# Kernel tuning notes

Hardware: AMD Instinct MI355X
Metric: run time of the kernel (lower is better)

Reference implementation:

```python
import jax, jax.numpy as jnp
import numpy as np
from jax import lax

B, CIN, COUT, H, W = 4, 32, 64, 192, 192
K = 3  # kernel size
RED = 16  # SE reduction
EPS = 1e-5


def _conv2d_same(x, w, b):
    y = lax.conv_general_dilated(x, w, (1, 1), 'SAME',
                                 dimension_numbers=('NCHW', 'OIHW', 'NCHW'))
    return y + b[None, :, None, None]


def _bilinear_gather(x, py, px):
    # x: [B,C,H,W]; py/px: [B,KK,H,W] absolute sample coords -> [B,C,KK,H,W]
    Bb, C, Hh, Ww = x.shape
    KK = py.shape[1]
    y0 = jnp.floor(py); x0 = jnp.floor(px)
    wy = py - y0; wx = px - x0
    x_flat = x.reshape(Bb, C, Hh * Ww)

    def corner(yi, xi, wgt):
        valid = (yi >= 0) & (yi < Hh) & (xi >= 0) & (xi < Ww)
        yc = jnp.clip(yi, 0, Hh - 1).astype(jnp.int32)
        xc = jnp.clip(xi, 0, Ww - 1).astype(jnp.int32)
        idx = (yc * Ww + xc).reshape(Bb, 1, KK * Hh * Ww)
        g = jnp.take_along_axis(x_flat, idx, axis=2).reshape(Bb, C, KK, Hh, Ww)
        w_eff = (wgt * valid.astype(x.dtype))[:, None]  # [B,1,KK,H,W]
        return g * w_eff

    out = (corner(y0, x0, (1 - wy) * (1 - wx))
           + corner(y0, x0 + 1, (1 - wy) * wx)
           + corner(y0 + 1, x0, wy * (1 - wx))
           + corner(y0 + 1, x0 + 1, wy * wx))
    return out  # [B,C,KK,H,W]


def _deform_conv(x, offsets, w, b):
    # torchvision DeformConv2d, stride 1, pad 1, dilation 1, 1 offset group.
    Bb, C, Hh, Ww = x.shape
    off = offsets.reshape(Bb, K * K, 2, Hh, Ww)
    dy, dx = off[:, :, 0], off[:, :, 1]  # [B,KK,H,W]
    ky, kx = jnp.meshgrid(jnp.arange(K) - 1, jnp.arange(K) - 1, indexing='ij')
    hg, wg = jnp.meshgrid(jnp.arange(Hh), jnp.arange(Ww), indexing='ij')
    py = hg[None, None] + ky.reshape(-1)[None, :, None, None] + dy
    px = wg[None, None] + kx.reshape(-1)[None, :, None, None] + dx
    sampled = _bilinear_gather(x, py, px)  # [B,CIN,KK,H,W]
    y = jnp.einsum('bckhw,ock->bohw', sampled, w.reshape(w.shape[0], C, K * K))
    return y + b[None, :, None, None]


def _forward(x, w_off, b_off, w_def, b_def, bn_gamma, bn_beta,
             fc1_w, fc1_b, fc2_w, fc2_b):
    offsets = _conv2d_same(x, w_off, b_off)
    y = _deform_conv(x, offsets, w_def, b_def)
    # BatchNorm2d (training-mode batch statistics)
    mean = jnp.mean(y, axis=(0, 2, 3), keepdims=True)
    var = jnp.var(y, axis=(0, 2, 3), keepdims=True)
    y = (y - mean) * lax.rsqrt(var + EPS)
    y = y * bn_gamma[None, :, None, None] + bn_beta[None, :, None, None]
    # SE layer
    s = jnp.mean(y, axis=(2, 3))  # [B,C]
    s = jax.nn.relu(s @ fc1_w.T + fc1_b)
    s = jax.nn.sigmoid(s @ fc2_w.T + fc2_b)
    y = y * s[:, :, None, None]
    y = jax.nn.relu(y)
    # MaxPool 2x2 stride 2
    y = lax.reduce_window(y, -jnp.inf, lax.max, (1, 1, 2, 2), (1, 1, 2, 2), 'VALID')
    return y


def setup_inputs() -> dict:
    key = jax.random.key(0)
    ks = jax.random.split(key, 12)
    rn = lambda k, s, sc=1.0: (jax.random.normal(k, s, dtype=jnp.float32) * sc)
    return {
        'x': rn(ks[0], (B, CIN, H, W)),
        'w_off': rn(ks[1], (2 * K * K, CIN, K, K), 0.02),
        'b_off': jnp.zeros((2 * K * K,), jnp.float32),
        'w_def': rn(ks[2], (COUT, CIN, K, K), 0.05),
        'b_def': rn(ks[3], (COUT,), 0.05),
        'bn_gamma': jnp.ones((COUT,), jnp.float32),
        'bn_beta': jnp.zeros((COUT,), jnp.float32),
        'fc1_w': rn(ks[4], (COUT // RED, COUT), 0.1),
        'fc1_b': jnp.zeros((COUT // RED,), jnp.float32),
        'fc2_w': rn(ks[5], (COUT, COUT // RED), 0.1),
        'fc2_b': jnp.zeros((COUT,), jnp.float32),
    }


def reference(x, w_off, b_off, w_def, b_def, bn_gamma, bn_beta,
              fc1_w, fc1_b, fc2_w, fc2_b):
    return _forward(x, w_off, b_off, w_def, b_def, bn_gamma, bn_beta,
                    fc1_w, fc1_b, fc2_w, fc2_b)
```

## Files before the change

### kernel.cpp

```cpp
#include <hip/hip_runtime.h>
#include <math.h>

#define B_    4
#define CIN_  32
#define COUT_ 64
#define H_    192
#define W_    192
#define HW_   (H_ * W_)
#define NPIX_ (B_ * HW_)
#define EPS_  1e-5f

static __device__ __forceinline__ int swz2304(int blk) {
    return ((blk & 7) * 288) + (blk >> 3);
}

struct Cr { int o00, o01, o10, o11; float w00, w01, w10, w11; };

__global__ __launch_bounds__(256) void k_pre(
    const float* __restrict__ x, const float* __restrict__ w_def,
    const float* __restrict__ w_off, float* __restrict__ xt,
    float* __restrict__ wt_def, float* __restrict__ wt_off,
    float* __restrict__ stats)
{
    if (blockIdx.x < NPIX_ / 256) {
        __shared__ float lds[32 * 257];
        const int tid  = threadIdx.x;
        const int pid0 = blockIdx.x * 256;
        const int b    = pid0 / HW_;
        const int rem0 = pid0 - b * HW_;
        const float* xb = x + (size_t)b * CIN_ * HW_ + rem0;

#pragma unroll
        for (int c = 0; c < 32; ++c)
            lds[c * 257 + tid] = xb[c * HW_ + tid];
        __syncthreads();

        float4* dst = (float4*)(xt + (size_t)pid0 * 32);
#pragma unroll
        for (int i = 0; i < 8; ++i) {
            const int idx = i * 256 + tid;
            const int px  = idx >> 3;
            const int q   = idx & 7;
            float4 v;
            v.x = lds[(q * 4 + 0) * 257 + px];
            v.y = lds[(q * 4 + 1) * 257 + px];
            v.z = lds[(q * 4 + 2) * 257 + px];
            v.w = lds[(q * 4 + 3) * 257 + px];
            dst[idx] = v;
        }
    } else {
        const int i = (blockIdx.x - NPIX_ / 256) * 256 + threadIdx.x;
        if (i < 18432) {
            const int o  = i & 63;
            const int c  = (i >> 6) & 31;
            const int kk = i >> 11;
            wt_def[i] = w_def[(o * 32 + c) * 9 + kk];
        } else if (i < 18432 + 5760) {
            const int e  = i - 18432;
            const int c  = e & 31;
            const int t  = e >> 5;
            const int o  = t % 20;
            const int kk = t / 20;
            wt_off[e] = (o < 18) ? w_off[(o * 32 + c) * 9 + kk] : 0.f;
        } else if (i < 18432 + 5760 + 512) {
            stats[i - 18432 - 5760] = 0.f;
        }
    }
}

__global__ __launch_bounds__(256, 6) void k_fused(
    const float* __restrict__ xt, const float* __restrict__ wto,
    const float* __restrict__ b_off, const float* __restrict__ wtd,
    const float* __restrict__ b_def, float* __restrict__ y,
    float* __restrict__ sum_bc, float* __restrict__ sumsq_bc)
{
    __shared__ __align__(16) float smem[6336];
    __shared__ float offlds[20 * 64];
    float4 (*tile)[198] = (float4(*)[198])smem;
    float* vbuf = smem;

    const int tid  = threadIdx.x;
    const int px   = tid & 63;
    const int og   = __builtin_amdgcn_readfirstlane(tid >> 6);
    const int lane = tid & 63;

    const int blk  = swz2304(blockIdx.x);
    const int base = blk * 64;
    const int b    = base / HW_;
    const int rem0 = base - b * HW_;
    const int h0   = rem0 / W_;
    const int w0   = rem0 - h0 * W_;
    const float* xb = xt + (size_t)b * HW_ * 32;

    for (int i = tid; i < 1584; i += 256) {
        const int j   = i & 7;
        const int rec = i >> 3;
        const int r   = rec / 66;
        const int cc  = rec - r * 66;
        const int hc  = min(max(h0 + r - 1, 0), H_ - 1);
        const int wc  = min(max(w0 + cc - 1, 0), W_ - 1);
        tile[j][rec] = *(const float4*)(xb + (hc * W_ + wc) * 32 + j * 4);
    }
    __syncthreads();

    {
        const bool rv0 = (h0 - 1 >= 0), rv2 = (h0 + 1 < H_);
        float acc5[5] = {0.f, 0.f, 0.f, 0.f, 0.f};
#pragma unroll 1
        for (int kk = 0; kk < 9; ++kk) {
            const int ky = kk / 3, kx = kk % 3;
            const bool rok = (ky == 0) ? rv0 : ((ky == 2) ? rv2 : true);
            const int wcol = w0 + px + kx - 1;
            const float g = (rok && wcol >= 0 && wcol < W_) ? 1.f : 0.f;
            const int rec = ky * 66 + px + kx;

            float4 v[8];
#pragma unroll
            for (int j = 0; j < 8; ++j) {
                v[j] = tile[j][rec];
                v[j].x *= g; v[j].y *= g; v[j].z *= g; v[j].w *= g;
            }
            const float* wk = wto + (kk * 20 + og * 5) * 32;
#pragma unroll
            for (int oo = 0; oo < 5; ++oo) {
                const float4* wr = (const float4*)(wk + oo * 32);
                float s = acc5[oo];
#pragma unroll
                for (int j = 0; j < 8; ++j) {
                    const float4 wv = wr[j];
                    s += v[j].x * wv.x + v[j].y * wv.y
                       + v[j].z * wv.z + v[j].w * wv.w;
                }
                acc5[oo] = s;
            }
        }
#pragma unroll
        for (int oo = 0; oo < 5; ++oo) {
            const int o = og * 5 + oo;
            if (o < 18) offlds[o * 64 + px] = acc5[oo] + b_off[o];
        }
    }
    __syncthreads();

    const int h = h0;
    const int w = w0 + px;
    const float* xg = xb + og * 8;

    float acc[16];
#pragma unroll
    for (int q = 0; q < 16; ++q) acc[q] = 0.f;

    auto mk = [&](int kk) -> Cr {
        const float dy = offlds[(2 * kk) * 64 + px];
        const float dx = offlds[(2 * kk + 1) * 64 + px];
        const float py = (float)(h + kk / 3 - 1) + dy;
        const float qx = (float)(w + kk % 3 - 1) + dx;
        const float y0f = floorf(py), x0f = floorf(qx);
        const float wy = py - y0f, wx = qx - x0f;
        const int iy0 = (int)y0f, ix0 = (int)x0f;
        const int iy1 = iy0 + 1,  ix1 = ix0 + 1;
        const float vy0 = (iy0 >= 0 && iy0 < H_) ? 1.f : 0.f;
        const float vy1 = (iy1 >= 0 && iy1 < H_) ? 1.f : 0.f;
        const float vx0 = (ix0 >= 0 && ix0 < W_) ? 1.f : 0.f;
        const float vx1 = (ix1 >= 0 && ix1 < W_) ? 1.f : 0.f;
        Cr c;
        c.w00 = (1.f - wy) * (1.f - wx) * vy0 * vx0;
        c.w01 = (1.f - wy) * wx * vy0 * vx1;
        c.w10 = wy * (1.f - wx) * vy1 * vx0;
        c.w11 = wy * wx * vy1 * vx1;
        const int cy0 = min(max(iy0, 0), H_ - 1), cy1 = min(max(iy1, 0), H_ - 1);
        const int cx0 = min(max(ix0, 0), W_ - 1), cx1 = min(max(ix1, 0), W_ - 1);
        c.o00 = (cy0 * W_ + cx0) * 32; c.o01 = (cy0 * W_ + cx1) * 32;
        c.o10 = (cy1 * W_ + cx0) * 32; c.o11 = (cy1 * W_ + cx1) * 32;
        return c;
    };

    {
        Cr c0 = mk(0);
        float4 A0 = *(const float4*)(xg + c0.o00), A1 = *(const float4*)(xg + c0.o00 + 4);
        float4 B0 = *(const float4*)(xg + c0.o01), B1 = *(const float4*)(xg + c0.o01 + 4);
        float4 C0 = *(const float4*)(xg + c0.o10), C1 = *(const float4*)(xg + c0.o10 + 4);
        float4 D0 = *(const float4*)(xg + c0.o11), D1 = *(const float4*)(xg + c0.o11 + 4);
        float v[8];
        v[0] = c0.w00 * A0.x + c0.w01 * B0.x + c0.w10 * C0.x + c0.w11 * D0.x;
        v[1] = c0.w00 * A0.y + c0.w01 * B0.y + c0.w10 * C0.y + c0.w11 * D0.y;
        v[2] = c0.w00 * A0.z + c0.w01 * B0.z + c0.w10 * C0.z + c0.w11 * D0.z;
        v[3] = c0.w00 * A0.w + c0.w01 * B0.w + c0.w10 * C0.w + c0.w11 * D0.w;
        v[4] = c0.w00 * A1.x + c0.w01 * B1.x + c0.w10 * C1.x + c0.w11 * D1.x;
        v[5] = c0.w00 * A1.y + c0.w01 * B1.y + c0.w10 * C1.y + c0.w11 * D1.y;
        v[6] = c0.w00 * A1.z + c0.w01 * B1.z + c0.w10 * C1.z + c0.w11 * D1.z;
        v[7] = c0.w00 * A1.w + c0.w01 * B1.w + c0.w10 * C1.w + c0.w11 * D1.w;
#pragma unroll
        for (int j = 0; j < 8; ++j) vbuf[(og * 8 + j) * 64 + px] = v[j];
    }
    __syncthreads();

#pragma unroll 1
    for (int kk = 0; kk < 9; ++kk) {
        Cr nx; float4 A0, A1, B0, B1, C0, C1, D0, D1;
        if (kk < 8) {
            nx = mk(kk + 1);
            A0 = *(const float4*)(xg + nx.o00); A1 = *(const float4*)(xg + nx.o00 + 4);
            B0 = *(const float4*)(xg + nx.o01); B1 = *(const float4*)(xg + nx.o01 + 4);
            C0 = *(const float4*)(xg + nx.o10); C1 = *(const float4*)(xg + nx.o10 + 4);
            D0 = *(const float4*)(xg + nx.o11); D1 = *(const float4*)(xg + nx.o11 + 4);
        }

        const float* vp = vbuf + (kk & 1) * 2048;
        const float* wk = wtd + (kk << 11) + (og << 4);
#pragma unroll 8
        for (int c = 0; c < 32; ++c) {
            const float vv = vp[c * 64 + px];
            const float4* wr = (const float4*)(wk + (c << 6));
            const float4 w0 = wr[0], w1 = wr[1], w2 = wr[2], w3 = wr[3];
            acc[ 0] += vv * w0.x; acc[ 1] += vv * w0.y;
            acc[ 2] += vv * w0.z; acc[ 3] += vv * w0.w;
            acc[ 4] += vv * w1.x; acc[ 5] += vv * w1.y;
            acc[ 6] += vv * w1.z; acc[ 7] += vv * w1.w;
            acc[ 8] += vv * w2.x; acc[ 9] += vv * w2.y;
            acc[10] += vv * w2.z; acc[11] += vv * w2.w;
            acc[12] += vv * w3.x; acc[13] += vv * w3.y;
            acc[14] += vv * w3.z; acc[15] += vv * w3.w;
        }

        if (kk < 8) {
            float v[8];
            v[0] = nx.w00 * A0.x + nx.w01 * B0.x + nx.w10 * C0.x + nx.w11 * D0.x;
            v[1] = nx.w00 * A0.y + nx.w01 * B0.y + nx.w10 * C0.y + nx.w11 * D0.y;
            v[2] = nx.w00 * A0.z + nx.w01 * B0.z + nx.w10 * C0.z + nx.w11 * D0.z;
            v[3] = nx.w00 * A0.w + nx.w01 * B0.w + nx.w10 * C0.w + nx.w11 * D0.w;
            v[4] = nx.w00 * A1.x + nx.w01 * B1.x + nx.w10 * C1.x + nx.w11 * D1.x;
            v[5] = nx.w00 * A1.y + nx.w01 * B1.y + nx.w10 * C1.y + nx.w11 * D1.y;
            v[6] = nx.w00 * A1.z + nx.w01 * B1.z + nx.w10 * C1.z + nx.w11 * D1.z;
            v[7] = nx.w00 * A1.w + nx.w01 * B1.w + nx.w10 * C1.w + nx.w11 * D1.w;
            float* wp = vbuf + ((kk + 1) & 1) * 2048;
#pragma unroll
            for (int j = 0; j < 8; ++j) wp[(og * 8 + j) * 64 + px] = v[j];
            __syncthreads();
        }
    }

    const int rem = rem0 + px;
    float* yp = y + ((size_t)b * COUT_ + og * 16) * HW_ + rem;
#pragma unroll
    for (int q = 0; q < 16; ++q) {
        acc[q] += b_def[og * 16 + q];
        yp[q * HW_] = acc[q];
    }

    float ls = 0.f, lq = 0.f;
#pragma unroll
    for (int o = 0; o < 16; ++o) {
        float t = acc[o];
        float u = t * t;
#pragma unroll
        for (int s = 32; s; s >>= 1) {
            t += __shfl_xor(t, s, 64);
            u += __shfl_xor(u, s, 64);
        }
        if (lane == o) { ls = t; lq = u; }
    }
    if (lane < 16) {
        atomicAdd(&sum_bc[b * 64 + og * 16 + lane], ls);
        atomicAdd(&sumsq_bc[b * 64 + og * 16 + lane], lq);
    }
}

__global__ __launch_bounds__(256) void k_finish(
    const float* __restrict__ y,
    const float* __restrict__ sum_bc, const float* __restrict__ sumsq_bc,
    const float* __restrict__ gamma, const float* __restrict__ beta,
    const float* __restrict__ fc1_w, const float* __restrict__ fc1_b,
    const float* __restrict__ fc2_w, const float* __restrict__ fc2_b,
    float* __restrict__ out)
{
    __shared__ float sal[256], sbb[256], sin_[256];
    const int tid = threadIdx.x;
    {
        const int b = tid >> 6, c = tid & 63;
        float ch_s = 0.f, ch_q = 0.f;
#pragma unroll
        for (int bb = 0; bb < 4; ++bb) {
            ch_s += sum_bc[bb * 64 + c];
            ch_q += sumsq_bc[bb * 64 + c];
        }
        const float invN = 1.f / (float)(B_ * HW_);
        const float mean = ch_s * invN;
        const float var  = ch_q * invN - mean * mean;
        const float a    = gamma[c] * rsqrtf(var + EPS_);
        const float bi   = beta[c] - mean * a;
        sin_[tid] = a * (sum_bc[tid] * (1.f / (float)HW_)) + bi;
        __syncthreads();
        float hv[4];
#pragma unroll
        for (int j = 0; j < 4; ++j) {
            float hs = fc1_b[j];
            for (int cc = 0; cc < 64; ++cc)
                hs += sin_[b * 64 + cc] * fc1_w[j * 64 + cc];
            hv[j] = fmaxf(hs, 0.f);
        }
        float o = fc2_b[c];
#pragma unroll
        for (int j = 0; j < 4; ++j) o += hv[j] * fc2_w[c * 4 + j];
        const float s = 1.f / (1.f + expf(-o));
        sal[tid] = a * s;
        sbb[tid] = bi * s;
    }
    __syncthreads();

    const int t    = blockIdx.x * 256 + tid;
    const int opix = t * 2;
    const int bc   = opix / (96 * 96);
    const int rem  = opix - bc * (96 * 96);
    const int oh   = rem / 96, ow = rem - oh * 96;
    const float al = sal[bc], bb = sbb[bc];
    const float* yp = y + (size_t)bc * HW_ + (2 * oh) * W_ + 2 * ow;
    const float4 r0 = *(const float4*)yp;
    const float4 r1 = *(const float4*)(yp + W_);
    float2 st;
    st.x = fmaxf(fmaxf(fmaxf(fmaf(r0.x, al, bb), fmaf(r0.y, al, bb)),
                       fmaxf(fmaf(r1.x, al, bb), fmaf(r1.y, al, bb))), 0.f);
    st.y = fmaxf(fmaxf(fmaxf(fmaf(r0.z, al, bb), fmaf(r0.w, al, bb)),
                       fmaxf(fmaf(r1.z, al, bb), fmaf(r1.w, al, bb))), 0.f);
    *(float2*)(out + opix) = st;
}

extern "C" void kernel_launch(void* const* d_in, const int* in_sizes, int n_in,
                              void* d_out, int out_size, void* d_ws, size_t ws_size,
                              hipStream_t stream)
{
    const float* x     = (const float*)d_in[0];
    const float* w_off = (const float*)d_in[1];
    const float* b_off = (const float*)d_in[2];
    const float* w_def = (const float*)d_in[3];
    const float* b_def = (const float*)d_in[4];
    const float* gamma = (const float*)d_in[5];
    const float* beta  = (const float*)d_in[6];
    const float* fc1_w = (const float*)d_in[7];
    const float* fc1_b = (const float*)d_in[8];
    const float* fc2_w = (const float*)d_in[9];
    const float* fc2_b = (const float*)d_in[10];
    float* out = (float*)d_out;

    float* ws   = (float*)d_ws;
    float* yb     = ws;
    float* xt     = yb + 9437184;
    float* wt_def = xt + 4718592;
    float* wt_off = wt_def + 18432;
    float* stats  = wt_off + 5760;
    float* sum_bc   = stats;
    float* sumsq_bc = stats + 256;

    k_pre   <<<dim3(NPIX_ / 256 + 97), dim3(256), 0, stream>>>(
                x, w_def, w_off, xt, wt_def, wt_off, stats);
    k_fused <<<dim3(NPIX_ / 64), dim3(256), 0, stream>>>(
                xt, wt_off, b_off, wt_def, b_def, yb, sum_bc, sumsq_bc);
    k_finish<<<dim3(B_ * COUT_ * 96 * 96 / 512), dim3(256), 0, stream>>>(
                yb, sum_bc, sumsq_bc, gamma, beta,
                fc1_w, fc1_b, fc2_w, fc2_b, out);
}
```

Baseline: 221.6 us.

## Compute deformable conv contraction with split-fp16 MFMA instead of scalar FMA

Replaces the per-thread scalar FMA loop over 32 channels × 16 outputs with MFMA 16x16x32 f16 instructions. Both activations and weights are split into hi/lo fp16 parts, and three products (hi·hi, lo·hi, hi·lo) are accumulated to keep near-fp32 accuracy. The work is remapped so each wavefront handles 16 pixels × 64 outputs with 8 channels per lane-quad. This removes the LDS double-buffer exchange of sampled values and the per-kk barriers. Each lane now gathers its own bilinear samples, with no software prefetch of the next tap. Occupancy is lowered to 4 blocks per CU, the statistics reduction is restructured, and weights are stored pre-swizzled in fp16 pairs.

```diff
diff --git a/kernel.cpp b/kernel.cpp
--- a/kernel.cpp
+++ b/kernel.cpp
@@ -10,16 +10,19 @@
 #define NPIX_ (B_ * HW_)
 #define EPS_  1e-5f
 
+typedef _Float16 half8 __attribute__((ext_vector_type(8)));
+typedef float    f32x4 __attribute__((ext_vector_type(4)));
+
+#define WTN_ 18432
+
 static __device__ __forceinline__ int swz2304(int blk) {
     return ((blk & 7) * 288) + (blk >> 3);
 }
-
-struct Cr { int o00, o01, o10, o11; float w00, w01, w10, w11; };
 
 __global__ __launch_bounds__(256) void k_pre(
     const float* __restrict__ x, const float* __restrict__ w_def,
     const float* __restrict__ w_off, float* __restrict__ xt,
-    float* __restrict__ wt_def, float* __restrict__ wt_off,
+    _Float16* __restrict__ wt_def, float* __restrict__ wt_off,
     float* __restrict__ stats)
 {
     if (blockIdx.x < NPIX_ / 256) {
@@ -50,34 +53,39 @@
         }
     } else {
         const int i = (blockIdx.x - NPIX_ / 256) * 256 + threadIdx.x;
-        if (i < 18432) {
-            const int o  = i & 63;
-            const int c  = (i >> 6) & 31;
+        if (i < WTN_) {
+            const int j  = i & 7;
+            const int ln = (i >> 3) & 63;
+            const int ot = (i >> 9) & 3;
             const int kk = i >> 11;
-            wt_def[i] = w_def[(o * 32 + c) * 9 + kk];
-        } else if (i < 18432 + 5760) {
-            const int e  = i - 18432;
+            const int o  = ot * 16 + (ln & 15);
+            const int c  = (ln >> 4) * 8 + j;
+            const float wv = w_def[(o * 32 + c) * 9 + kk];
+            const _Float16 hi = (_Float16)wv;
+            wt_def[i]        = hi;
+            wt_def[WTN_ + i] = (_Float16)(wv - (float)hi);
+        } else if (i < WTN_ + 5760) {
+            const int e  = i - WTN_;
             const int c  = e & 31;
             const int t  = e >> 5;
             const int o  = t % 20;
             const int kk = t / 20;
             wt_off[e] = (o < 18) ? w_off[(o * 32 + c) * 9 + kk] : 0.f;
-        } else if (i < 18432 + 5760 + 512) {
-            stats[i - 18432 - 5760] = 0.f;
-        }
-    }
-}
-
-__global__ __launch_bounds__(256, 6) void k_fused(
+        } else if (i < WTN_ + 5760 + 512) {
+            stats[i - WTN_ - 5760] = 0.f;
+        }
+    }
+}
+
+__global__ __launch_bounds__(256, 4) void k_fused(
     const float* __restrict__ xt, const float* __restrict__ wto,
-    const float* __restrict__ b_off, const float* __restrict__ wtd,
+    const float* __restrict__ b_off, const _Float16* __restrict__ wtd,
     const float* __restrict__ b_def, float* __restrict__ y,
     float* __restrict__ sum_bc, float* __restrict__ sumsq_bc)
 {
     __shared__ __align__(16) float smem[6336];
-    __shared__ float offlds[20 * 64];
     float4 (*tile)[198] = (float4(*)[198])smem;
-    float* vbuf = smem;
+    float* offlds = smem;
 
     const int tid  = threadIdx.x;
     const int px   = tid & 63;
@@ -103,9 +111,9 @@
     }
     __syncthreads();
 
+    float acc5[5] = {0.f, 0.f, 0.f, 0.f, 0.f};
     {
         const bool rv0 = (h0 - 1 >= 0), rv2 = (h0 + 1 < H_);
-        float acc5[5] = {0.f, 0.f, 0.f, 0.f, 0.f};
 #pragma unroll 1
         for (int kk = 0; kk < 9; ++kk) {
             const int ky = kk / 3, kx = kk % 3;
@@ -134,27 +142,44 @@
                 acc5[oo] = s;
             }
         }
-#pragma unroll
-        for (int oo = 0; oo < 5; ++oo) {
-            const int o = og * 5 + oo;
-            if (o < 18) offlds[o * 64 + px] = acc5[oo] + b_off[o];
-        }
     }
     __syncthreads();
-
-    const int h = h0;
-    const int w = w0 + px;
-    const float* xg = xb + og * 8;
-
-    float acc[16];
-#pragma unroll
-    for (int q = 0; q < 16; ++q) acc[q] = 0.f;
-
-    auto mk = [&](int kk) -> Cr {
-        const float dy = offlds[(2 * kk) * 64 + px];
-        const float dx = offlds[(2 * kk + 1) * 64 + px];
-        const float py = (float)(h + kk / 3 - 1) + dy;
-        const float qx = (float)(w + kk % 3 - 1) + dx;
+#pragma unroll
+    for (int oo = 0; oo < 5; ++oo) {
+        const int o = og * 5 + oo;
+        if (o < 18) offlds[o * 64 + px] = acc5[oo] + b_off[o];
+    }
+    __syncthreads();
+
+    const int l15 = lane & 15;
+    const int lq4 = lane >> 4;
+    const int pxl = (og << 4) + l15;
+    const int wc_ = w0 + pxl;
+    const float* xg = xb + lq4 * 8;
+    const _Float16* wbh = wtd + lane * 8;
+    const _Float16* wbl = wtd + WTN_ + lane * 8;
+
+    f32x4 acc[4];
+#pragma unroll
+    for (int ot = 0; ot < 4; ++ot) acc[ot] = (f32x4){0.f, 0.f, 0.f, 0.f};
+
+#pragma unroll 1
+    for (int kk = 0; kk < 9; ++kk) {
+        const _Float16* wkh = wbh + (kk << 11);
+        const _Float16* wkl = wbl + (kk << 11);
+        const half8 bh0 = *(const half8*)(wkh);
+        const half8 bh1 = *(const half8*)(wkh + 512);
+        const half8 bh2 = *(const half8*)(wkh + 1024);
+        const half8 bh3 = *(const half8*)(wkh + 1536);
+        const half8 bl0 = *(const half8*)(wkl);
+        const half8 bl1 = *(const half8*)(wkl + 512);
+        const half8 bl2 = *(const half8*)(wkl + 1024);
+        const half8 bl3 = *(const half8*)(wkl + 1536);
+
+        const float dy = offlds[(2 * kk) * 64 + pxl];
+        const float dx = offlds[(2 * kk + 1) * 64 + pxl];
+        const float py = (float)(h0 + kk / 3 - 1) + dy;
+        const float qx = (float)(wc_ + kk % 3 - 1) + dx;
         const float y0f = floorf(py), x0f = floorf(qx);
         const float wy = py - y0f, wx = qx - x0f;
         const int iy0 = (int)y0f, ix0 = (int)x0f;
@@ -163,107 +188,72 @@
         const float vy1 = (iy1 >= 0 && iy1 < H_) ? 1.f : 0.f;
         const float vx0 = (ix0 >= 0 && ix0 < W_) ? 1.f : 0.f;
         const float vx1 = (ix1 >= 0 && ix1 < W_) ? 1.f : 0.f;
-        Cr c;
-        c.w00 = (1.f - wy) * (1.f - wx) * vy0 * vx0;
-        c.w01 = (1.f - wy) * wx * vy0 * vx1;
-        c.w10 = wy * (1.f - wx) * vy1 * vx0;
-        c.w11 = wy * wx * vy1 * vx1;
+        const float w00 = (1.f - wy) * (1.f - wx) * vy0 * vx0;
+        const float w01 = (1.f - wy) * wx * vy0 * vx1;
+        const float w10 = wy * (1.f - wx) * vy1 * vx0;
+        const float w11 = wy * wx * vy1 * vx1;
         const int cy0 = min(max(iy0, 0), H_ - 1), cy1 = min(max(iy1, 0), H_ - 1);
         const int cx0 = min(max(ix0, 0), W_ - 1), cx1 = min(max(ix1, 0), W_ - 1);
-        c.o00 = (cy0 * W_ + cx0) * 32; c.o01 = (cy0 * W_ + cx1) * 32;
-        c.o10 = (cy1 * W_ + cx0) * 32; c.o11 = (cy1 * W_ + cx1) * 32;
-        return c;
-    };
-
-    {
-        Cr c0 = mk(0);
-        float4 A0 = *(const float4*)(xg + c0.o00), A1 = *(const float4*)(xg + c0.o00 + 4);
-        float4 B0 = *(const float4*)(xg + c0.o01), B1 = *(const float4*)(xg + c0.o01 + 4);
-        float4 C0 = *(const float4*)(xg + c0.o10), C1 = *(const float4*)(xg + c0.o10 + 4);
-        float4 D0 = *(const float4*)(xg + c0.o11), D1 = *(const float4*)(xg + c0.o11 + 4);
+        const int o00 = (cy0 * W_ + cx0) * 32, o01 = (cy0 * W_ + cx1) * 32;
+        const int o10 = (cy1 * W_ + cx0) * 32, o11 = (cy1 * W_ + cx1) * 32;
+
+        const float4 A0 = *(const float4*)(xg + o00), A1 = *(const float4*)(xg + o00 + 4);
+        const float4 B0 = *(const float4*)(xg + o01), B1 = *(const float4*)(xg + o01 + 4);
+        const float4 C0 = *(const float4*)(xg + o10), C1 = *(const float4*)(xg + o10 + 4);
+        const float4 D0 = *(const float4*)(xg + o11), D1 = *(const float4*)(xg + o11 + 4);
+
         float v[8];
-        v[0] = c0.w00 * A0.x + c0.w01 * B0.x + c0.w10 * C0.x + c0.w11 * D0.x;
-        v[1] = c0.w00 * A0.y + c0.w01 * B0.y + c0.w10 * C0.y + c0.w11 * D0.y;
-        v[2] = c0.w00 * A0.z + c0.w01 * B0.z + c0.w10 * C0.z + c0.w11 * D0.z;
-        v[3] = c0.w00 * A0.w + c0.w01 * B0.w + c0.w10 * C0.w + c0.w11 * D0.w;
-        v[4] = c0.w00 * A1.x + c0.w01 * B1.x + c0.w10 * C1.x + c0.w11 * D1.x;
-        v[5] = c0.w00 * A1.y + c0.w01 * B1.y + c0.w10 * C1.y + c0.w11 * D1.y;
-        v[6] = c0.w00 * A1.z + c0.w01 * B1.z + c0.w10 * C1.z + c0.w11 * D1.z;
-        v[7] = c0.w00 * A1.w + c0.w01 * B1.w + c0.w10 * C1.w + c0.w11 * D1.w;
-#pragma unroll
-        for (int j = 0; j < 8; ++j) vbuf[(og * 8 + j) * 64 + px] = v[j];
-    }
-    __syncthreads();
-
-#pragma unroll 1
-    for (int kk = 0; kk < 9; ++kk) {
-        Cr nx; float4 A0, A1, B0, B1, C0, C1, D0, D1;
-        if (kk < 8) {
-            nx = mk(kk + 1);
-            A0 = *(const float4*)(xg + nx.o00); A1 = *(const float4*)(xg + nx.o00 + 4);
-            B0 = *(const float4*)(xg + nx.o01); B1 = *(const float4*)(xg + nx.o01 + 4);
-            C0 = *(const float4*)(xg + nx.o10); C1 = *(const float4*)(xg + nx.o10 + 4);
-            D0 = *(const float4*)(xg + nx.o11); D1 = *(const float4*)(xg + nx.o11 + 4);
-        }
-
-        const float* vp = vbuf + (kk & 1) * 2048;
-        const float* wk = wtd + (kk << 11) + (og << 4);
-#pragma unroll 8
-        for (int c = 0; c < 32; ++c) {
-            const float vv = vp[c * 64 + px];
-            const float4* wr = (const float4*)(wk + (c << 6));
-            const float4 w0 = wr[0], w1 = wr[1], w2 = wr[2], w3 = wr[3];
-            acc[ 0] += vv * w0.x; acc[ 1] += vv * w0.y;
-            acc[ 2] += vv * w0.z; acc[ 3] += vv * w0.w;
-            acc[ 4] += vv * w1.x; acc[ 5] += vv * w1.y;
-            acc[ 6] += vv * w1.z; acc[ 7] += vv * w1.w;
-            acc[ 8] += vv * w2.x; acc[ 9] += vv * w2.y;
-            acc[10] += vv * w2.z; acc[11] += vv * w2.w;
-            acc[12] += vv * w3.x; acc[13] += vv * w3.y;
-            acc[14] += vv * w3.z; acc[15] += vv * w3.w;
-        }
-
-        if (kk < 8) {
-            float v[8];
-            v[0] = nx.w00 * A0.x + nx.w01 * B0.x + nx.w10 * C0.x + nx.w11 * D0.x;
-            v[1] = nx.w00 * A0.y + nx.w01 * B0.y + nx.w10 * C0.y + nx.w11 * D0.y;
-            v[2] = nx.w00 * A0.z + nx.w01 * B0.z + nx.w10 * C0.z + nx.w11 * D0.z;
-            v[3] = nx.w00 * A0.w + nx.w01 * B0.w + nx.w10 * C0.w + nx.w11 * D0.w;
-            v[4] = nx.w00 * A1.x + nx.w01 * B1.x + nx.w10 * C1.x + nx.w11 * D1.x;
-            v[5] = nx.w00 * A1.y + nx.w01 * B1.y + nx.w10 * C1.y + nx.w11 * D1.y;
-            v[6] = nx.w00 * A1.z + nx.w01 * B1.z + nx.w10 * C1.z + nx.w11 * D1.z;
-            v[7] = nx.w00 * A1.w + nx.w01 * B1.w + nx.w10 * C1.w + nx.w11 * D1.w;
-            float* wp = vbuf + ((kk + 1) & 1) * 2048;
-#pragma unroll
-            for (int j = 0; j < 8; ++j) wp[(og * 8 + j) * 64 + px] = v[j];
-            __syncthreads();
-        }
-    }
-
-    const int rem = rem0 + px;
-    float* yp = y + ((size_t)b * COUT_ + og * 16) * HW_ + rem;
-#pragma unroll
-    for (int q = 0; q < 16; ++q) {
-        acc[q] += b_def[og * 16 + q];
-        yp[q * HW_] = acc[q];
-    }
-
-    float ls = 0.f, lq = 0.f;
-#pragma unroll
-    for (int o = 0; o < 16; ++o) {
-        float t = acc[o];
-        float u = t * t;
-#pragma unroll
-        for (int s = 32; s; s >>= 1) {
-            t += __shfl_xor(t, s, 64);
-            u += __shfl_xor(u, s, 64);
-        }
-        if (lane == o) { ls = t; lq = u; }
-    }
-    if (lane < 16) {
-        atomicAdd(&sum_bc[b * 64 + og * 16 + lane], ls);
-        atomicAdd(&sumsq_bc[b * 64 + og * 16 + lane], lq);
-    }
+        v[0] = w00 * A0.x + w01 * B0.x + w10 * C0.x + w11 * D0.x;
+        v[1] = w00 * A0.y + w01 * B0.y + w10 * C0.y + w11 * D0.y;
+        v[2] = w00 * A0.z + w01 * B0.z + w10 * C0.z + w11 * D0.z;
+        v[3] = w00 * A0.w + w01 * B0.w + w10 * C0.w + w11 * D0.w;
+        v[4] = w00 * A1.x + w01 * B1.x + w10 * C1.x + w11 * D1.x;
+        v[5] = w00 * A1.y + w01 * B1.y + w10 * C1.y + w11 * D1.y;
+        v[6] = w00 * A1.z + w01 * B1.z + w10 * C1.z + w11 * D1.z;
+        v[7] = w00 * A1.w + w01 * B1.w + w10 * C1.w + w11 * D1.w;
+
+        half8 a_hi, a_lo;
+#pragma unroll
+        for (int j = 0; j < 8; ++j) {
+            const _Float16 h = (_Float16)v[j];
+            a_hi[j] = h;
+            a_lo[j] = (_Float16)(v[j] - (float)h);
+        }
+
+        acc[0] = __builtin_amdgcn_mfma_f32_16x16x32_f16(a_hi, bh0, acc[0], 0, 0, 0);
+        acc[1] = __builtin_amdgcn_mfma_f32_16x16x32_f16(a_hi, bh1, acc[1], 0, 0, 0);
+        acc[2] = __builtin_amdgcn_mfma_f32_16x16x32_f16(a_hi, bh2, acc[2], 0, 0, 0);
+        acc[3] = __builtin_amdgcn_mfma_f32_16x16x32_f16(a_hi, bh3, acc[3], 0, 0, 0);
+        acc[0] = __builtin_amdgcn_mfma_f32_16x16x32_f16(a_lo, bh0, acc[0], 0, 0, 0);
+        acc[1] = __builtin_amdgcn_mfma_f32_16x16x32_f16(a_lo, bh1, acc[1], 0, 0, 0);
+        acc[2] = __builtin_amdgcn_mfma_f32_16x16x32_f16(a_lo, bh2, acc[2], 0, 0, 0);
+        acc[3] = __builtin_amdgcn_mfma_f32_16x16x32_f16(a_lo, bh3, acc[3], 0, 0, 0);
+        acc[0] = __builtin_amdgcn_mfma_f32_16x16x32_f16(a_hi, bl0, acc[0], 0, 0, 0);
+        acc[1] = __builtin_amdgcn_mfma_f32_16x16x32_f16(a_hi, bl1, acc[1], 0, 0, 0);
+        acc[2] = __builtin_amdgcn_mfma_f32_16x16x32_f16(a_hi, bl2, acc[2], 0, 0, 0);
+        acc[3] = __builtin_amdgcn_mfma_f32_16x16x32_f16(a_hi, bl3, acc[3], 0, 0, 0);
+    }
+
+    const int rem = rem0 + (og << 4) + (lq4 << 2);
+    float sred[4], qred[4];
+#pragma unroll
+    for (int ot = 0; ot < 4; ++ot) {
+        const float bias = b_def[ot * 16 + l15];
+        f32x4 av = acc[ot];
+        av[0] += bias; av[1] += bias; av[2] += bias; av[3] += bias;
+        *(f32x4*)(y + ((size_t)(b * COUT_ + ot * 16 + l15)) * HW_ + rem) = av;
+        float s = av[0] + av[1] + av[2] + av[3];
+        float q = av[0] * av[0] + av[1] * av[1] + av[2] * av[2] + av[3] * av[3];
+        s += __shfl_xor(s, 16, 64); s += __shfl_xor(s, 32, 64);
+        q += __shfl_xor(q, 16, 64); q += __shfl_xor(q, 32, 64);
+        sred[ot] = s; qred[ot] = q;
+    }
+    float ms = sred[0], mq = qred[0];
+    if (lq4 == 1)      { ms = sred[1]; mq = qred[1]; }
+    else if (lq4 == 2) { ms = sred[2]; mq = qred[2]; }
+    else if (lq4 == 3) { ms = sred[3]; mq = qred[3]; }
+    atomicAdd(&sum_bc[b * COUT_ + lane], ms);
+    atomicAdd(&sumsq_bc[b * COUT_ + lane], mq);
 }
 
 __global__ __launch_bounds__(256) void k_finish(
@@ -343,13 +333,13 @@
     float* out = (float*)d_out;
 
     float* ws   = (float*)d_ws;
-    float* yb     = ws;
-    float* xt     = yb + 9437184;
-    float* wt_def = xt + 4718592;
-    float* wt_off = wt_def + 18432;
-    float* stats  = wt_off + 5760;
-    float* sum_bc   = stats;
-    float* sumsq_bc = stats + 256;
+    float* yb        = ws;
+    float* xt        = yb + 9437184;
+    _Float16* wt_def = (_Float16*)(xt + 4718592);
+    float* wt_off    = xt + 4718592 + 18432;
+    float* stats     = wt_off + 5760;
+    float* sum_bc    = stats;
+    float* sumsq_bc  = stats + 256;
 
     k_pre   <<<dim3(NPIX_ / 256 + 97), dim3(256), 0, stream>>>(
                 x, w_def, w_off, xt, wt_def, wt_off, stats);
```

Result: slower. 249.7 us (+12.7%).
